# Kernel tuning notes

Hardware: AMD Instinct MI355X
Metric: run time of the kernel (lower is better)

Reference implementation:

```python
import jax, jax.numpy as jnp
import numpy as np

N_CONST = 188
P = 16
HIDDEN = 128
DE = 5
DO = 6
N_TARGETS = 5
BATCH = 32


def _edge_indices(n):
    # receiver/sender pairs in the same order as itertools.product, skipping diagonal
    r, s = np.meshgrid(np.arange(n), np.arange(n), indexing='ij')
    mask = r != s
    return jnp.asarray(r[mask]), jnp.asarray(s[mask])  # each [n*(n-1)]


def _linear_params(key, fan_in, fan_out):
    kw, kb = jax.random.split(key)
    w = jax.random.normal(kw, (fan_in, fan_out), jnp.float32) / np.sqrt(fan_in)
    b = jax.random.normal(kb, (fan_out,), jnp.float32) * 0.01
    return w, b


def setup_inputs() -> dict:
    key = jax.random.key(0)
    ks = jax.random.split(key, 10)
    inp = {"x": jax.random.normal(ks[0], (BATCH, N_CONST, P), jnp.float32)}
    h2 = HIDDEN // 2
    dims = [
        ("fr1", 2 * P, HIDDEN), ("fr2", HIDDEN, h2), ("fr3", h2, DE),
        ("fo1", P + DE, HIDDEN), ("fo2", HIDDEN, h2), ("fo3", h2, DO),
        ("fc1", DO * N_CONST, HIDDEN), ("fc2", HIDDEN, h2), ("fc3", h2, N_TARGETS),
    ]
    for i, (name, fi, fo) in enumerate(dims):
        w, b = _linear_params(ks[i + 1], fi, fo)
        inp[name + "_w"] = w
        inp[name + "_b"] = b
    return inp


def reference(x, fr1_w, fr1_b, fr2_w, fr2_b, fr3_w, fr3_b,
              fo1_w, fo1_b, fo2_w, fo2_b, fo3_w, fo3_b,
              fc1_w, fc1_b, fc2_w, fc2_b, fc3_w, fc3_b):
    B, n, p = x.shape
    recv, send = _edge_indices(n)  # [Nr]
    # gather receiver/sender node features (replaces one-hot matmuls with Rr, Rs)
    e_in = jnp.concatenate([x[:, recv], x[:, send]], axis=-1)  # [B, Nr, 2P]
    h = jax.nn.relu(e_in @ fr1_w + fr1_b)
    h = jax.nn.relu(h @ fr2_w + fr2_b)
    E = jax.nn.relu(h @ fr3_w + fr3_b)  # [B, Nr, De]
    # scatter-add edge effects back to receiver nodes (replaces E @ Rr^T)
    Ebar = jnp.zeros((B, n, E.shape[-1]), x.dtype).at[:, recv].add(E)  # [B, N, De]
    c = jnp.concatenate([x, Ebar], axis=-1)  # [B, N, P+De]
    h = jax.nn.relu(c @ fo1_w + fo1_b)
    h = jax.nn.relu(h @ fo2_w + fo2_b)
    O = jax.nn.relu(h @ fo3_w + fo3_b)  # [B, N, Do]
    h = jax.nn.relu(O.reshape(B, -1) @ fc1_w + fc1_b)
    h = jax.nn.relu(h @ fc2_w + fc2_b)
    return h @ fc3_w + fc3_b  # [B, n_targets]
```

## Files before the change

kernel.cpp:

```cpp
#include <hip/hip_runtime.h>

#define BB   32
#define NN   188
#define PP   16
#define HID  128
#define HH2  64
#define DE   5
#define DO   6
#define NT   5
#define ROWS_O (BB*NN)
#define RT   32
#define KO   (PP+DE)

typedef __attribute__((ext_vector_type(8))) short short8;
typedef __attribute__((ext_vector_type(4))) float float4_;
typedef __attribute__((ext_vector_type(4))) unsigned uint4_;

__device__ __forceinline__ short f2bf(float v) {
    union { float f; unsigned u; } a; a.f = v;
    unsigned r = a.u + 0x7fff + ((a.u >> 16) & 1);
    return (short)(r >> 16);
}
__device__ __forceinline__ unsigned r2u(float v) {
    v = v > 0.f ? v : 0.f;
    return __float_as_uint(v) + 0x8000u;
}
__device__ __forceinline__ unsigned pack_hi16(unsigned hi, unsigned lo) {
    return __builtin_amdgcn_perm(hi, lo, 0x07060302);
}

#define XB_OFF    0
#define XB_ELTS   (BB*NN*24)
#define W1T_OFF   (XB_OFF + XB_ELTS)
#define W1T_ELTS  (HID*40)
#define W2S_OFF   (W1T_OFF + W1T_ELTS)
#define W2S_ELTS  (16*64*8)
#define W3S_OFF   (W2S_OFF + W2S_ELTS)
#define W3S_ELTS  (2*64*8)
#define SHORT_TOTAL (W3S_OFF + W3S_ELTS)

__device__ __forceinline__ int kmap(int q, int e) {
    return (e < 4) ? (q*4 + e) : (16 + q*4 + (e - 4));
}

__global__ void prep_kernel(const float* __restrict__ x,
                            const float* __restrict__ w1,
                            const float* __restrict__ w2,
                            const float* __restrict__ w3,
                            short* __restrict__ ws)
{
    const int i = blockIdx.x * blockDim.x + threadIdx.x;
    const int stride = gridDim.x * blockDim.x;
    for (int idx = i; idx < BB*NN*PP; idx += stride) {
        int row = idx >> 4, k = idx & 15;
        ws[XB_OFF + row*24 + k] = f2bf(x[idx]);
    }
    for (int idx = i; idx < 32*HID; idx += stride) {
        int k = idx >> 7, n = idx & 127;
        ws[W1T_OFF + n*40 + k] = f2bf(w1[idx]);
    }
    for (int idx = i; idx < W2S_ELTS; idx += stride) {
        int f = idx >> 9;
        int l = (idx >> 3) & 63;
        int e = idx & 7;
        int tt = f >> 2, s = f & 3;
        int q = l >> 4, n16 = l & 15;
        int k = 32*s + kmap(q, e);
        int n = tt*16 + n16;
        ws[W2S_OFF + idx] = f2bf(w2[k*HH2 + n]);
    }
    for (int idx = i; idx < W3S_ELTS; idx += stride) {
        int s2 = idx >> 9;
        int l = (idx >> 3) & 63;
        int e = idx & 7;
        int q = l >> 4, n16 = l & 15;
        int k = 32*s2 + kmap(q, e);
        ws[W3S_OFF + idx] = (n16 < DE) ? f2bf(w3[k*DE + n16]) : (short)0;
    }
}

__global__ __launch_bounds__(256)
void edge_mfma_kernel(const short* __restrict__ ws_s,
                      const float* __restrict__ b1,
                      const float* __restrict__ b2,
                      const float* __restrict__ b3,
                      float* __restrict__ ebar)
{
    const short* xb  = ws_s + XB_OFF;
    const short* w1t = ws_s + W1T_OFF;
    const short* w3g = ws_s + W3S_OFF;

    __shared__ __align__(16) unsigned wsmem[4096];
    __shared__ __align__(16) float sB1[HID];
    __shared__ float red[4][16];

    const int bi   = blockIdx.x;
    const int b    = bi / NN;
    const int recv = bi - b*NN;
    const int tid  = threadIdx.x;
    const int wave = tid >> 6;
    const int lane = tid & 63;
    const int n16  = lane & 15;
    const int q    = lane >> 4;

    {
        const uint4* src = (const uint4*)(ws_s + W2S_OFF);
        uint4* dst = (uint4*)wsmem;
        #pragma unroll
        for (int i = 0; i < 4; ++i) dst[tid + i*256] = src[tid + i*256];
    }
    if (tid < HID) sB1[tid] = b1[tid];

    short8 W1f[8];
    #pragma unroll
    for (int t = 0; t < 8; ++t)
        W1f[t] = *(const short8*)(w1t + (t*16 + n16)*40 + q*8);
    short8 W3f[2];
    #pragma unroll
    for (int s = 0; s < 2; ++s)
        W3f[s] = *(const short8*)(w3g + s*512 + lane*8);
    float4_ bias2v[4];
    #pragma unroll
    for (int tt = 0; tt < 4; ++tt)
        bias2v[tt] = *(const float4_*)(b2 + tt*16 + q*4);
    float4_ bias3r;
    #pragma unroll
    for (int rg = 0; rg < 4; ++rg) {
        int o = q*4 + rg;
        bias3r[rg] = (o < DE) ? b3[o] : 0.f;
    }

    __syncthreads();

    const short* w2l = (const short*)wsmem;
    const short* xrow = xb + b*(NN*24);

    float acc[4] = {0.f, 0.f, 0.f, 0.f};

    #pragma unroll
    for (int ti = 0; ti < 3; ++ti) {
        const int rowbase = (wave*3 + ti) * 16;
        const int e = rowbase + n16;
        int send = e + (e >= recv ? 1 : 0);
        if (send > NN-1) send = NN-1;
        const int node = (q < 2) ? recv : send;
        short8 E1 = *(const short8*)(xrow + node*24 + (q & 1)*8);

        float4_ C2[4];
        #pragma unroll
        for (int tt = 0; tt < 4; ++tt) C2[tt] = bias2v[tt];

        #pragma unroll
        for (int s = 0; s < 4; ++s) {
            float4_ cb0 = *(const float4_*)(sB1 + (2*s)*16   + q*4);
            float4_ cb1 = *(const float4_*)(sB1 + (2*s+1)*16 + q*4);
            float4_ Ca = __builtin_amdgcn_mfma_f32_16x16x32_bf16(W1f[2*s],   E1, cb0, 0, 0, 0);
            float4_ Cb = __builtin_amdgcn_mfma_f32_16x16x32_bf16(W1f[2*s+1], E1, cb1, 0, 0, 0);
            uint4_ dv = (uint4_){ pack_hi16(r2u(Ca[1]), r2u(Ca[0])),
                                  pack_hi16(r2u(Ca[3]), r2u(Ca[2])),
                                  pack_hi16(r2u(Cb[1]), r2u(Cb[0])),
                                  pack_hi16(r2u(Cb[3]), r2u(Cb[2])) };
            short8 Bf = __builtin_bit_cast(short8, dv);
            #pragma unroll
            for (int tt = 0; tt < 4; ++tt) {
                short8 A2 = *(const short8*)(w2l + (tt*4 + s)*512 + lane*8);
                C2[tt] = __builtin_amdgcn_mfma_f32_16x16x32_bf16(A2, Bf, C2[tt], 0, 0, 0);
            }
        }

        float4_ C3 = bias3r;
        #pragma unroll
        for (int s2 = 0; s2 < 2; ++s2) {
            float4_ Cc = C2[2*s2], Cd = C2[2*s2+1];
            uint4_ dv = (uint4_){ pack_hi16(r2u(Cc[1]), r2u(Cc[0])),
                                  pack_hi16(r2u(Cc[3]), r2u(Cc[2])),
                                  pack_hi16(r2u(Cd[1]), r2u(Cd[0])),
                                  pack_hi16(r2u(Cd[3]), r2u(Cd[2])) };
            short8 B3f = __builtin_bit_cast(short8, dv);
            C3 = __builtin_amdgcn_mfma_f32_16x16x32_bf16(W3f[s2], B3f, C3, 0, 0, 0);
        }
        const bool ok = (e < NN-1);
        #pragma unroll
        for (int rg = 0; rg < 4; ++rg) {
            float v = C3[rg];
            v = v > 0.f ? v : 0.f;
            acc[rg] += ok ? v : 0.f;
        }
    }

    #pragma unroll
    for (int rg = 0; rg < 4; ++rg) {
        acc[rg] += __shfl_xor(acc[rg], 1);
        acc[rg] += __shfl_xor(acc[rg], 2);
        acc[rg] += __shfl_xor(acc[rg], 4);
        acc[rg] += __shfl_xor(acc[rg], 8);
    }
    if (n16 == 0) {
        #pragma unroll
        for (int rg = 0; rg < 4; ++rg) red[wave][q*4 + rg] = acc[rg];
    }
    __syncthreads();
    if (wave == 0 && lane < DE) {
        float tot = red[0][lane] + red[1][lane] + red[2][lane] + red[3][lane];
        ebar[bi*DE + lane] = tot;
    }
}

__global__ __launch_bounds__(512)
void obj_mlp_kernel(const float* __restrict__ x, const float* __restrict__ ebar,
                    const float* __restrict__ w1, const float* __restrict__ b1,
                    const float* __restrict__ w2, const float* __restrict__ b2,
                    const float* __restrict__ w3, const float* __restrict__ b3,
                    float* __restrict__ o_out)
{
    __shared__ float sW[HID*HH2];
    __shared__ float sB1[HID];
    __shared__ float sB2[HH2];
    __shared__ float sCin[RT*KO];
    __shared__ float sH1[RT*HID];
    __shared__ float sH2t[HH2*(RT+1)];
    const int tid = threadIdx.x;
    const int rbase = blockIdx.x * RT;

    for (int i = tid; i < KO*HID; i += 512) sW[i] = w1[i];
    if (tid < HID) sB1[tid] = b1[tid];
    else if (tid < HID+HH2) sB2[tid-HID] = b2[tid-HID];
    for (int i = tid; i < RT*KO; i += 512) {
        int r = i / KO, k = i - r*KO;
        int gr = rbase + r;
        int b = gr / NN;
        int node = gr - b*NN;
        sCin[i] = (k < PP) ? x[(b*NN+node)*PP + k]
                           : ebar[(b*NN+node)*DE + (k-PP)];
    }
    __syncthreads();

    {
        const int j = tid & (HID-1);
        const int g = tid >> 7;
        float w[KO];
        #pragma unroll
        for (int k = 0; k < KO; ++k) w[k] = sW[k*HID + j];
        const float bj = sB1[j];
        #pragma unroll
        for (int rr = 0; rr < 8; ++rr) {
            const int r = g*8 + rr;
            const float* e = &sCin[r*KO];
            float a0=0.f,a1=0.f,a2=0.f;
            #pragma unroll
            for (int k = 0; k < KO; k += 3) {
                a0 += w[k+0]*e[k+0];
                a1 += w[k+1]*e[k+1];
                a2 += w[k+2]*e[k+2];
            }
            float v = a0+a1+a2+bj;
            sH1[r*HID + j] = v > 0.f ? v : 0.f;
        }
    }
    __syncthreads();
    for (int i = tid; i < HID*HH2; i += 512) sW[i] = w2[i];
    __syncthreads();

    {
        const int j = tid & (HH2-1);
        const int g = tid >> 6;
        float acc[4];
        #pragma unroll
        for (int rr = 0; rr < 4; ++rr) acc[rr] = sB2[j];
        #pragma unroll
        for (int kc = 0; kc < HID; kc += 32) {
            float w[32];
            #pragma unroll
            for (int kk = 0; kk < 32; ++kk) w[kk] = sW[(kc+kk)*HH2 + j];
            #pragma unroll
            for (int rr = 0; rr < 4; ++rr) {
                const float* h = &sH1[(g*4+rr)*HID + kc];
                float a0=0.f,a1=0.f,a2=0.f,a3=0.f;
                #pragma unroll
                for (int kk = 0; kk < 32; kk += 4) {
                    a0 += w[kk+0]*h[kk+0];
                    a1 += w[kk+1]*h[kk+1];
                    a2 += w[kk+2]*h[kk+2];
                    a3 += w[kk+3]*h[kk+3];
                }
                acc[rr] += (a0+a1)+(a2+a3);
            }
        }
        #pragma unroll
        for (int rr = 0; rr < 4; ++rr) {
            float v = acc[rr];
            sH2t[j*(RT+1) + (g*4+rr)] = v > 0.f ? v : 0.f;
        }
    }
    __syncthreads();

    if (tid < RT*DO) {
        const int r = tid & (RT-1);
        const int c = tid >> 5;
        float a0=0.f,a1=0.f,a2=0.f,a3=0.f;
        #pragma unroll
        for (int k = 0; k < HH2; k += 4) {
            a0 += sH2t[(k+0)*(RT+1)+r]*w3[(k+0)*DO+c];
            a1 += sH2t[(k+1)*(RT+1)+r]*w3[(k+1)*DO+c];
            a2 += sH2t[(k+2)*(RT+1)+r]*w3[(k+2)*DO+c];
            a3 += sH2t[(k+3)*(RT+1)+r]*w3[(k+3)*DO+c];
        }
        float v = (a0+a1)+(a2+a3) + b3[c];
        v = v > 0.f ? v : 0.f;
        int gr = rbase + r;
        int b = gr / NN;
        int node = gr - b*NN;
        o_out[b*(NN*DO) + node*DO + c] = v;
    }
}

__global__ __launch_bounds__(256)
void fc_kernel(const float* __restrict__ o_in,
               const float* __restrict__ w1, const float* __restrict__ b1,
               const float* __restrict__ w2, const float* __restrict__ b2,
               const float* __restrict__ w3, const float* __restrict__ b3,
               float* __restrict__ out)
{
    __shared__ __align__(16) float s_in[NN*DO];
    __shared__ float s_p[256];
    __shared__ float s_h1[HID];
    __shared__ float s_h2[HH2];
    const int b = blockIdx.x, tid = threadIdx.x;

    for (int i = tid; i < NN*DO; i += 256) s_in[i] = o_in[b*(NN*DO) + i];
    __syncthreads();

    {
        const int j = tid & (HID-1);
        const int h = tid >> 7;
        const float4* s4 = (const float4*)&s_in[h*564];
        const float* wbase = w1 + (size_t)(h*564)*HID + j;
        float a0=0.f,a1=0.f,a2=0.f,a3=0.f;
        #pragma unroll 4
        for (int i = 0; i < 141; ++i) {
            float4 v = s4[i];
            const float* wp = wbase + (size_t)i*4*HID;
            a0 += v.x * wp[0];
            a1 += v.y * wp[HID];
            a2 += v.z * wp[2*HID];
            a3 += v.w * wp[3*HID];
        }
        s_p[tid] = (a0+a1)+(a2+a3);
    }
    __syncthreads();
    if (tid < HID) {
        float v = s_p[tid] + s_p[tid+HID] + b1[tid];
        s_h1[tid] = v > 0.f ? v : 0.f;
    }
    __syncthreads();

    {
        const int j = tid & (HH2-1);
        const int q = tid >> 6;
        float acc = 0.f;
        #pragma unroll
        for (int kk = 0; kk < 32; ++kk) {
            int k = q*32 + kk;
            acc += s_h1[k] * w2[k*HH2 + j];
        }
        s_p[tid] = acc;
    }
    __syncthreads();
    if (tid < HH2) {
        float v = s_p[tid] + s_p[tid+64] + s_p[tid+128] + s_p[tid+192] + b2[tid];
        s_h2[tid] = v > 0.f ? v : 0.f;
    }
    __syncthreads();

    if (tid < NT) {
        float acc = b3[tid];
        #pragma unroll
        for (int k = 0; k < HH2; ++k)
            acc += s_h2[k] * w3[k*NT + tid];
        out[b*NT + tid] = acc;
    }
}

extern "C" void kernel_launch(void* const* d_in, const int* in_sizes, int n_in,
                              void* d_out, int out_size, void* d_ws, size_t ws_size,
                              hipStream_t stream) {
    (void)in_sizes; (void)n_in; (void)out_size; (void)ws_size;
    const float* x     = (const float*)d_in[0];
    const float* fr1_w = (const float*)d_in[1];
    const float* fr1_b = (const float*)d_in[2];
    const float* fr2_w = (const float*)d_in[3];
    const float* fr2_b = (const float*)d_in[4];
    const float* fr3_w = (const float*)d_in[5];
    const float* fr3_b = (const float*)d_in[6];
    const float* fo1_w = (const float*)d_in[7];
    const float* fo1_b = (const float*)d_in[8];
    const float* fo2_w = (const float*)d_in[9];
    const float* fo2_b = (const float*)d_in[10];
    const float* fo3_w = (const float*)d_in[11];
    const float* fo3_b = (const float*)d_in[12];
    const float* fc1_w = (const float*)d_in[13];
    const float* fc1_b = (const float*)d_in[14];
    const float* fc2_w = (const float*)d_in[15];
    const float* fc2_b = (const float*)d_in[16];
    const float* fc3_w = (const float*)d_in[17];
    const float* fc3_b = (const float*)d_in[18];

    short* ws_s = (short*)d_ws;
    size_t fbase = ((size_t)SHORT_TOTAL*2 + 15) & ~(size_t)15;
    float* ebar = (float*)((char*)d_ws + fbase);
    float* o_ws = ebar + BB*NN*DE;

    prep_kernel<<<128, 256, 0, stream>>>(x, fr1_w, fr2_w, fr3_w, ws_s);
    edge_mfma_kernel<<<BB*NN, 256, 0, stream>>>(ws_s, fr1_b, fr2_b, fr3_b, ebar);
    obj_mlp_kernel<<<ROWS_O/RT, 512, 0, stream>>>(
        x, ebar, fo1_w, fo1_b, fo2_w, fo2_b, fo3_w, fo3_b, o_ws);
    fc_kernel<<<BB, 256, 0, stream>>>(
        o_ws, fc1_w, fc1_b, fc2_w, fc2_b, fc3_w, fc3_b, (float*)d_out);
}
```

Baseline: 171.2 us.

## Assign one receiver per wave in edge kernel with prefetched gathers

The edge kernel now maps each wave to a separate receiver node, with four receivers per block, instead of splitting one receiver's 187 edges across four waves. The grid shrinks by four, so the per-block staging of W2 into shared memory and the register loads of W1/W3 are amortised over four times as much work. The cross-wave shared-memory reduction and its barrier are gone, and each wave writes its sums directly. The loop runs 12 tiles per wave and prefetches the next tile's node features before computing the current one, trading fewer, longer-running blocks for less setup overhead and synchronisation.

```diff
diff --git a/kernel.cpp b/kernel.cpp
--- a/kernel.cpp
+++ b/kernel.cpp
@@ -92,16 +92,15 @@
 
     __shared__ __align__(16) unsigned wsmem[4096];
     __shared__ __align__(16) float sB1[HID];
-    __shared__ float red[4][16];
-
-    const int bi   = blockIdx.x;
-    const int b    = bi / NN;
-    const int recv = bi - b*NN;
+
     const int tid  = threadIdx.x;
     const int wave = tid >> 6;
     const int lane = tid & 63;
     const int n16  = lane & 15;
     const int q    = lane >> 4;
+    const int bi   = blockIdx.x * 4 + wave;
+    const int b    = bi / NN;
+    const int recv = bi - b*NN;
 
     {
         const uint4* src = (const uint4*)(ws_s + W2S_OFF);
@@ -134,17 +133,27 @@
 
     const short* w2l = (const short*)wsmem;
     const short* xrow = xb + b*(NN*24);
+    const bool rside = (q < 2);
 
     float acc[4] = {0.f, 0.f, 0.f, 0.f};
 
-    #pragma unroll
-    for (int ti = 0; ti < 3; ++ti) {
-        const int rowbase = (wave*3 + ti) * 16;
-        const int e = rowbase + n16;
-        int send = e + (e >= recv ? 1 : 0);
-        if (send > NN-1) send = NN-1;
-        const int node = (q < 2) ? recv : send;
-        short8 E1 = *(const short8*)(xrow + node*24 + (q & 1)*8);
+    short8 E1;
+    {
+        int send0 = n16 + (n16 >= recv ? 1 : 0);
+        const int node = rside ? recv : send0;
+        E1 = *(const short8*)(xrow + node*24 + (q & 1)*8);
+    }
+
+    #pragma unroll 2
+    for (int ti = 0; ti < 12; ++ti) {
+        short8 E1c = E1;
+        if (ti < 11) {
+            int en = (ti+1)*16 + n16;
+            int send = en + (en >= recv ? 1 : 0);
+            if (send > NN-1) send = NN-1;
+            const int node = rside ? recv : send;
+            E1 = *(const short8*)(xrow + node*24 + (q & 1)*8);
+        }
 
         float4_ C2[4];
         #pragma unroll
@@ -154,8 +163,8 @@
         for (int s = 0; s < 4; ++s) {
             float4_ cb0 = *(const float4_*)(sB1 + (2*s)*16   + q*4);
             float4_ cb1 = *(const float4_*)(sB1 + (2*s+1)*16 + q*4);
-            float4_ Ca = __builtin_amdgcn_mfma_f32_16x16x32_bf16(W1f[2*s],   E1, cb0, 0, 0, 0);
-            float4_ Cb = __builtin_amdgcn_mfma_f32_16x16x32_bf16(W1f[2*s+1], E1, cb1, 0, 0, 0);
+            float4_ Ca = __builtin_amdgcn_mfma_f32_16x16x32_bf16(W1f[2*s],   E1c, cb0, 0, 0, 0);
+            float4_ Cb = __builtin_amdgcn_mfma_f32_16x16x32_bf16(W1f[2*s+1], E1c, cb1, 0, 0, 0);
             uint4_ dv = (uint4_){ pack_hi16(r2u(Ca[1]), r2u(Ca[0])),
                                   pack_hi16(r2u(Ca[3]), r2u(Ca[2])),
                                   pack_hi16(r2u(Cb[1]), r2u(Cb[0])),
@@ -179,6 +188,7 @@
             short8 B3f = __builtin_bit_cast(short8, dv);
             C3 = __builtin_amdgcn_mfma_f32_16x16x32_bf16(W3f[s2], B3f, C3, 0, 0, 0);
         }
+        const int e = ti*16 + n16;
         const bool ok = (e < NN-1);
         #pragma unroll
         for (int rg = 0; rg < 4; ++rg) {
@@ -197,12 +207,10 @@
     }
     if (n16 == 0) {
         #pragma unroll
-        for (int rg = 0; rg < 4; ++rg) red[wave][q*4 + rg] = acc[rg];
-    }
-    __syncthreads();
-    if (wave == 0 && lane < DE) {
-        float tot = red[0][lane] + red[1][lane] + red[2][lane] + red[3][lane];
-        ebar[bi*DE + lane] = tot;
+        for (int rg = 0; rg < 4; ++rg) {
+            int o = q*4 + rg;
+            if (o < DE) ebar[bi*DE + o] = acc[rg];
+        }
     }
 }
 
@@ -411,7 +419,7 @@
     float* o_ws = ebar + BB*NN*DE;
 
     prep_kernel<<<128, 256, 0, stream>>>(x, fr1_w, fr2_w, fr3_w, ws_s);
-    edge_mfma_kernel<<<BB*NN, 256, 0, stream>>>(ws_s, fr1_b, fr2_b, fr3_b, ebar);
+    edge_mfma_kernel<<<(BB*NN)/4, 256, 0, stream>>>(ws_s, fr1_b, fr2_b, fr3_b, ebar);
     obj_mlp_kernel<<<ROWS_O/RT, 512, 0, stream>>>(
         x, ebar, fo1_w, fo1_b, fo2_w, fo2_b, fo3_w, fo3_b, o_ws);
     fc_kernel<<<BB, 256, 0, stream>>>(
```

Result: no change. 171.7 us (+0.3%).
